# Kernel tuning notes

Measured on AMD Instinct MI355X. Metric: run time of the kernel, lower is better.

Reference implementation:

```python
import jax, jax.numpy as jnp
import numpy as np

B, N, D_IN, D_OUT = 8, 2048, 128, 64
NEG_INF = -9e15
LEAKY_ALPHA = 0.2


def setup_inputs() -> dict:
    key = jax.random.key(0)
    k_h, k_adj, k_w, k_a = jax.random.split(key, 4)
    h = jax.random.normal(k_h, (B, N, D_IN), dtype=jnp.float32)
    # sparse-ish 0/1 adjacency with forced self-loops (diagonal ones)
    adj = (jax.random.uniform(k_adj, (B, N, N)) < 0.02).astype(jnp.float32)
    adj = jnp.maximum(adj, jnp.eye(N, dtype=jnp.float32)[None, :, :])
    # glorot uniform init for w and a
    lim_w = np.sqrt(6.0 / (D_IN + D_OUT))
    w = jax.random.uniform(k_w, (D_IN, D_OUT), minval=-lim_w, maxval=lim_w, dtype=jnp.float32)
    lim_a = np.sqrt(6.0 / (2 * D_OUT + 1))
    a = jax.random.uniform(k_a, (2 * D_OUT, 1), minval=-lim_a, maxval=lim_a, dtype=jnp.float32)
    return {"h": h, "adj": adj, "w": w, "a": a}


def reference(h, adj, w, a):
    # wh: (B, N, D_OUT)
    wh = jnp.einsum('bnd,df->bnf', h, w)
    # Split a into the halves acting on source (i) and target (j) features.
    # concat([wh_i, wh_j]) @ a == wh_i @ a1 + wh_j @ a2  (exact same math,
    # avoids materializing the (B,N,N,2F) pairwise tensor).
    f = wh.shape[-1]
    s1 = wh @ a[:f, 0]   # (B, N) -> score contribution of node i (rows)
    s2 = wh @ a[f:, 0]   # (B, N) -> score contribution of node j (cols)
    scores = s1[:, :, None] + s2[:, None, :]            # (B, N, N)
    scores = jnp.where(scores >= 0, scores, LEAKY_ALPHA * scores)  # LeakyReLU(0.2)
    masked = jnp.where(adj > 0, scores, NEG_INF)
    coeffs = jax.nn.softmax(masked, axis=2)             # (B, N, N)
    new_h = jnp.einsum('bij,bjf->bif', coeffs, wh)      # (B, N, D_OUT)
    return new_h
```

## Files before the change

kernel.cpp:

```cpp
#include <hip/hip_runtime.h>
#include <hip/hip_bf16.h>
#include <math.h>


#define GAT_B 8
#define GAT_N 2048
#define GAT_DIN 128
#define GAT_DOUT 64

__global__ __launch_bounds__(256) void gat_wh_kernel(
    const float* __restrict__ h, const float* __restrict__ w,
    const float* __restrict__ a, float* __restrict__ wh,
    float* __restrict__ s1, float* __restrict__ s2) {
  __shared__ float w_lds[GAT_DIN * GAT_DOUT];
  __shared__ float h_lds[4][GAT_DIN];

  for (int t = threadIdx.x; t < (GAT_DIN * GAT_DOUT) / 4; t += 256)
    ((float4*)w_lds)[t] = ((const float4*)w)[t];

  const int lane = threadIdx.x & 63;
  const int wv = threadIdx.x >> 6;
  const float a1 = a[lane];
  const float a2 = a[GAT_DOUT + lane];

  const int ngroups = (GAT_B * GAT_N) / 4;
  for (int rg = blockIdx.x; rg < ngroups; rg += gridDim.x) {
    __syncthreads();
    const float4* hsrc = (const float4*)(h + (size_t)rg * 4 * GAT_DIN);
    for (int t = threadIdx.x; t < (4 * GAT_DIN) / 4; t += 256)
      ((float4*)&h_lds[0][0])[t] = hsrc[t];
    __syncthreads();

    const int row = rg * 4 + wv;
    float acc = 0.f;
#pragma unroll 16
    for (int d = 0; d < GAT_DIN; ++d)
      acc = fmaf(h_lds[wv][d], w_lds[d * GAT_DOUT + lane], acc);

    wh[(size_t)row * GAT_DOUT + lane] = acc;

    float t1 = acc * a1, t2 = acc * a2;
#pragma unroll
    for (int off = 32; off >= 1; off >>= 1) {
      t1 += __shfl_xor(t1, off);
      t2 += __shfl_xor(t2, off);
    }
    if (lane == 0) { s1[row] = t1; s2[row] = t2; }
  }
}

__global__ __launch_bounds__(256) void gat_row_kernel(
    const float* __restrict__ adj, const float* __restrict__ wh,
    const float* __restrict__ s1, const float* __restrict__ s2,
    float* __restrict__ out) {
  const int lane = threadIdx.x & 63;
  const int wv = threadIdx.x >> 6;
  const int row = blockIdx.x * 4 + wv;
  const int b = row >> 11;

  const float* adj_row = adj + (size_t)row * GAT_N;
  const float* s2b = s2 + (size_t)b * GAT_N;
  const float* whb = wh + (size_t)b * GAT_N * GAT_DOUT;
  const float s1i = s1[row];

  float m = -INFINITY;
  float l = 0.f;
  float acc = 0.f;

  for (int c = 0; c < GAT_N; c += 256) {
    const float4 av = *(const float4*)(adj_row + c + lane * 4);
    const float4 sv = *(const float4*)(s2b + c + lane * 4);
#pragma unroll
    for (int comp = 0; comp < 4; ++comp) {
      const float a_c = (comp == 0) ? av.x : (comp == 1) ? av.y
                       : (comp == 2) ? av.z : av.w;
      const float s_c = (comp == 0) ? sv.x : (comp == 1) ? sv.y
                       : (comp == 2) ? sv.z : sv.w;
      unsigned long long msk = __ballot(a_c > 0.f);
      while (msk) {
        const int bit = __builtin_ctzll(msk);
        msk &= msk - 1;
        const float s2j = __shfl(s_c, bit);
        const int j = c + bit * 4 + comp;
        float sc = s1i + s2j;
        sc = (sc >= 0.f) ? sc : 0.2f * sc;
        if (sc > m) {
          const float r = __expf(m - sc);
          acc *= r;
          l *= r;
          m = sc;
        }
        const float e = __expf(sc - m);
        l += e;
        acc = fmaf(e, whb[(size_t)j * GAT_DOUT + lane], acc);
      }
    }
  }
  out[(size_t)row * GAT_DOUT + lane] = acc / l;
}

extern "C" void kernel_launch(void* const* d_in, const int* in_sizes, int n_in,
                              void* d_out, int out_size, void* d_ws, size_t ws_size,
                              hipStream_t stream) {
  const float* h   = (const float*)d_in[0];
  const float* adj = (const float*)d_in[1];
  const float* w   = (const float*)d_in[2];
  const float* a   = (const float*)d_in[3];
  float* out = (float*)d_out;

  const size_t rows = (size_t)GAT_B * GAT_N;
  float* wh = (float*)d_ws;
  float* s1 = wh + rows * GAT_DOUT;
  float* s2 = s1 + rows;

  gat_wh_kernel<<<1024, 256, 0, stream>>>(h, w, a, wh, s1, s2);

  gat_row_kernel<<<(GAT_B * GAT_N) / 4, 256, 0, stream>>>(adj, wh, s1, s2, out);
}
```

Baseline: 65.82 us.

## Compact nonzero neighbors into LDS per chunk and use chunk-level online softmax

Each wave now computes the LeakyReLU score in parallel for all 256 columns of a chunk, stream-compacts the nonzero-adjacency indices and scores into LDS using ballot plus mbcnt prefix, and takes a chunk max reduction. It then rescales once per chunk instead of doing a per-neighbor max/rescale branch with a serial shuffle. The gather loop is unrolled by two with independent accumulators to expose more memory-level parallelism. The cost is extra LDS traffic, 8KB of shared memory per block, and a wave reduction per chunk.

```diff
diff --git a/kernel.cpp b/kernel.cpp
--- a/kernel.cpp
+++ b/kernel.cpp
@@ -53,6 +53,9 @@
     const float* __restrict__ adj, const float* __restrict__ wh,
     const float* __restrict__ s1, const float* __restrict__ s2,
     float* __restrict__ out) {
+  __shared__ unsigned int idx_l[4][256];
+  __shared__ float sc_l[4][256];
+
   const int lane = threadIdx.x & 63;
   const int wv = threadIdx.x >> 6;
   const int row = blockIdx.x * 4 + wv;
@@ -62,41 +65,70 @@
   const float* s2b = s2 + (size_t)b * GAT_N;
   const float* whb = wh + (size_t)b * GAT_N * GAT_DOUT;
   const float s1i = s1[row];
+  unsigned int* my_idx = idx_l[wv];
+  float* my_sc = sc_l[wv];
 
-  float m = -INFINITY;
-  float l = 0.f;
-  float acc = 0.f;
+  float m = -1e30f;
+  float l0 = 0.f, l1 = 0.f;
+  float acc0 = 0.f, acc1 = 0.f;
 
   for (int c = 0; c < GAT_N; c += 256) {
     const float4 av = *(const float4*)(adj_row + c + lane * 4);
     const float4 sv = *(const float4*)(s2b + c + lane * 4);
+    int base = 0;
+    float cmax = -1e30f;
 #pragma unroll
     for (int comp = 0; comp < 4; ++comp) {
       const float a_c = (comp == 0) ? av.x : (comp == 1) ? av.y
                        : (comp == 2) ? av.z : av.w;
       const float s_c = (comp == 0) ? sv.x : (comp == 1) ? sv.y
                        : (comp == 2) ? sv.z : sv.w;
-      unsigned long long msk = __ballot(a_c > 0.f);
-      while (msk) {
-        const int bit = __builtin_ctzll(msk);
-        msk &= msk - 1;
-        const float s2j = __shfl(s_c, bit);
-        const int j = c + bit * 4 + comp;
-        float sc = s1i + s2j;
-        sc = (sc >= 0.f) ? sc : 0.2f * sc;
-        if (sc > m) {
-          const float r = __expf(m - sc);
-          acc *= r;
-          l *= r;
-          m = sc;
+      float sc = s1i + s_c;
+      sc = (sc >= 0.f) ? sc : 0.2f * sc;
+      const bool pred = a_c > 0.f;
+      const unsigned long long msk = __ballot(pred);
+      if (msk) {
+        const int prefix = __builtin_amdgcn_mbcnt_hi(
+            (unsigned)(msk >> 32),
+            __builtin_amdgcn_mbcnt_lo((unsigned)msk, 0u));
+        if (pred) {
+          my_idx[base + prefix] = (unsigned)(c + lane * 4 + comp);
+          my_sc[base + prefix] = sc;
+          cmax = fmaxf(cmax, sc);
         }
-        const float e = __expf(sc - m);
-        l += e;
-        acc = fmaf(e, whb[(size_t)j * GAT_DOUT + lane], acc);
+        base += (int)__popcll(msk);
       }
     }
+    if (base == 0) continue;
+
+#pragma unroll
+    for (int off = 32; off >= 1; off >>= 1)
+      cmax = fmaxf(cmax, __shfl_xor(cmax, off));
+
+    const float newm = fmaxf(m, cmax);
+    const float r = __expf(m - newm);
+    l0 *= r; l1 *= r; acc0 *= r; acc1 *= r;
+    m = newm;
+
+    int t = 0;
+    for (; t + 2 <= base; t += 2) {
+      const float e0 = __expf(my_sc[t] - m);
+      const float e1 = __expf(my_sc[t + 1] - m);
+      const unsigned j0 = my_idx[t];
+      const unsigned j1 = my_idx[t + 1];
+      l0 += e0;
+      l1 += e1;
+      acc0 = fmaf(e0, whb[(size_t)j0 * GAT_DOUT + lane], acc0);
+      acc1 = fmaf(e1, whb[(size_t)j1 * GAT_DOUT + lane], acc1);
+    }
+    if (t < base) {
+      const float e0 = __expf(my_sc[t] - m);
+      const unsigned j0 = my_idx[t];
+      l0 += e0;
+      acc0 = fmaf(e0, whb[(size_t)j0 * GAT_DOUT + lane], acc0);
+    }
   }
-  out[(size_t)row * GAT_DOUT + lane] = acc / l;
+  out[(size_t)row * GAT_DOUT + lane] = (acc0 + acc1) / (l0 + l1);
 }
 
 extern "C" void kernel_launch(void* const* d_in, const int* in_sizes, int n_in,
@@ -114,6 +146,5 @@
   float* s2 = s1 + rows;
 
   gat_wh_kernel<<<1024, 256, 0, stream>>>(h, w, a, wh, s1, s2);
-
   gat_row_kernel<<<(GAT_B * GAT_N) / 4, 256, 0, stream>>>(adj, wh, s1, s2, out);
 }
```

Result: faster. 64.16 us (-2.5%).
